# Performance work log

Measured on AMD Instinct MI355X. Metric: run time of the kernel, lower is better.

Reference implementation:

```python
import jax, jax.numpy as jnp
import numpy as np

BS, L, H, HD, R, HID = 4, 2048, 12, 64, 16, 768


def setup_inputs() -> dict:
    key = jax.random.key(0)
    k0, k1, k2, k3 = jax.random.split(key, 4)
    xavier = np.sqrt(2.0 / (H + HD))  # xavier_normal_ on (H, HD)
    lin = 1.0 / np.sqrt(HID)
    return {
        "hidden_states": jax.random.normal(k0, (BS, L, HID), jnp.float32),
        "K1_w": jax.random.normal(k1, (HID, H * HD), jnp.float32) * lin,
        "K1_b": jnp.zeros((H * HD,), jnp.float32),
        "V1_w": jax.random.normal(k2, (HID, H * HD), jnp.float32) * lin,
        "V1_b": jnp.zeros((H * HD,), jnp.float32),
        "ReadingHead": jax.random.normal(k3, (H, HD), jnp.float32) * xavier,
        "bidirection_weight": jnp.full((1, 1, H, 1, 2 * R), 1.0 / (2 * R), jnp.float32),
    }


def _scan_mmap(valid_mask, reverse):
    # valid_mask: (bs, L, H) bool. Sequential register-shift scan over positions 1..L-1.
    bs, Ln, Hn = valid_mask.shape
    idxs = jnp.arange(1, Ln, dtype=jnp.int32)
    masks = jnp.swapaxes(valid_mask[:, 1:], 0, 1)  # (L-1, bs, H)
    if reverse:
        idxs = idxs[::-1]
        masks = masks[::-1]
    init = jnp.zeros((bs, R + 1, Hn), jnp.int32)

    def step(valids, xm):
        i, m = xm
        valids = valids.at[:, 0].set(i)  # slot 0 <- current index (matches in-place torch order)
        shifted = jnp.where(m[:, None, :], valids[:, :-1], valids[:, 1:])
        valids = valids.at[:, 1:].set(shifted)
        return valids, valids[:, 1:]

    _, out = jax.lax.scan(step, init, (idxs, masks))  # (L-1, bs, R, H)
    if reverse:
        out = out[::-1]
    out = jnp.concatenate([jnp.zeros((1, bs, R, Hn), jnp.int32), out], axis=0)
    return jnp.swapaxes(out, 0, 1)  # (bs, L, R, H)


def reference(hidden_states, K1_w, K1_b, V1_w, V1_b, ReadingHead, bidirection_weight):
    K1 = jax.nn.relu(hidden_states @ K1_w + K1_b).reshape(BS, L, H, HD)
    V1 = jax.nn.relu(hidden_states @ V1_w + V1_b).reshape(BS, L, H, HD)
    dot_products = jnp.einsum('blhn,hn->blh', K1, ReadingHead)
    valid_mask = dot_products > 0.5  # attn_var default branch
    fm = _scan_mmap(valid_mask, False).reshape(BS, L * R, H)
    bm = _scan_mmap(valid_mask, True).reshape(BS, L * R, H)
    V_forward = jnp.take_along_axis(V1, fm[..., None], axis=1).reshape(BS, L, R, H, HD)
    V_backward = jnp.take_along_axis(V1, bm[..., None], axis=1).reshape(BS, L, R, H, HD)
    w = bidirection_weight[0, 0, :, 0, :]  # (H, 2R); first R -> forward, last R -> backward
    ctx = (jnp.einsum('blrhd,hr->blhd', V_forward, w[:, :R])
           + jnp.einsum('blrhd,hr->blhd', V_backward, w[:, R:]))
    return ctx.reshape(BS, L, H * HD)
```

## Files before the change

### kernel.cpp

```cpp
#include <hip/hip_runtime.h>
#include <hip/hip_bf16.h>

#define BS 4
#define L 2048
#define H 12
#define HD 64
#define R 16
#define HID 768
#define MARGIN 0.02f
#define FIXCAP 16384
#define FIXGRID 1024

typedef __attribute__((ext_vector_type(8))) short s8v;
typedef __attribute__((ext_vector_type(4))) float f32x4;

typedef __attribute__((address_space(1))) const void as1_void;
typedef __attribute__((address_space(3))) void as3_void;
#define GLOAD_LDS16(g, l) \
    __builtin_amdgcn_global_load_lds((as1_void*)(g), (as3_void*)(l), 16, 0, 0)

static __device__ __forceinline__ unsigned short f2bf_bits(float f) {
    __hip_bfloat16 h = __float2bfloat16(f);
    return *reinterpret_cast<unsigned short*>(&h);
}

__global__ __launch_bounds__(256) void convert_hs(
    const float* __restrict__ in, __hip_bfloat16* __restrict__ out,
    int* __restrict__ fixcnt)
{
    if (blockIdx.x == 0 && threadIdx.x == 0) *fixcnt = 0;
    int i = (blockIdx.x * 256 + threadIdx.x) * 4;
    float4 v = *(const float4*)&in[i];
    ushort4 o;
    o.x = f2bf_bits(v.x); o.y = f2bf_bits(v.y);
    o.z = f2bf_bits(v.z); o.w = f2bf_bits(v.w);
    *(ushort4*)&out[i] = o;
}

__global__ __launch_bounds__(256) void transpose_wt2(
    const float* __restrict__ K1w, const float* __restrict__ V1w,
    __hip_bfloat16* __restrict__ WtK, __hip_bfloat16* __restrict__ WtV)
{
    const float* in = blockIdx.z ? V1w : K1w;
    __hip_bfloat16* out = blockIdx.z ? WtV : WtK;
    __shared__ float s[32][33];
    const int c = threadIdx.x & 31, r8 = threadIdx.x >> 5;
    const int kt = blockIdx.x * 32, nt = blockIdx.y * 32;
#pragma unroll
    for (int rr = 0; rr < 4; ++rr) {
        int k = r8 + rr * 8;
        s[k][c] = in[(size_t)(kt + k) * HID + nt + c];
    }
    __syncthreads();
#pragma unroll
    for (int rr = 0; rr < 4; ++rr) {
        int n = r8 + rr * 8;
        out[(size_t)(nt + n) * HID + kt + c] = __float2bfloat16(s[c][n]);
    }
}

__global__ __launch_bounds__(256) void gemm_fused(
    const __hip_bfloat16* __restrict__ A,
    const __hip_bfloat16* __restrict__ WtK,
    const __hip_bfloat16* __restrict__ WtV,
    const float* __restrict__ K1b,
    const float* __restrict__ V1b,
    const float* __restrict__ RH,
    float* __restrict__ dots,
    int* __restrict__ fixlist,
    int* __restrict__ fixcnt,
    __hip_bfloat16* __restrict__ C)
{
    __shared__ alignas(16) __hip_bfloat16 As[128 * 32];
    __shared__ alignas(16) __hip_bfloat16 Bs[128 * 32];

    const int tid = threadIdx.x;
    const bool isV = blockIdx.y < 6;
    const int m0 = blockIdx.x * 128;
    const int n0 = (isV ? blockIdx.y : blockIdx.y - 6) * 128;
    const __hip_bfloat16* Bt = isV ? WtV : WtK;

    const int wid = tid >> 6, lane = tid & 63;
    const int quad = lane >> 4, lm = lane & 15;
    const int wm = wid & 1, wn = wid >> 1;

    const int rsub = lane >> 2;
    const int csw  = (lane & 3) ^ ((lane >> 3) & 3);
    const __hip_bfloat16* gA0 =
        A + (size_t)(m0 + 32 * wid + rsub) * HID + csw * 8;
    const __hip_bfloat16* gA1 = gA0 + (size_t)16 * HID;
    const __hip_bfloat16* gB0 =
        Bt + (size_t)(n0 + 32 * wid + rsub) * HID + csw * 8;
    const __hip_bfloat16* gB1 = gB0 + (size_t)16 * HID;
    __hip_bfloat16* lA0 = &As[(32 * wid) * 32];
    __hip_bfloat16* lA1 = &As[(32 * wid + 16) * 32];
    __hip_bfloat16* lB0 = &Bs[(32 * wid) * 32];
    __hip_bfloat16* lB1 = &Bs[(32 * wid + 16) * 32];

    const int fsw = (lm >> 1) & 3;
    const __hip_bfloat16* pA = &As[(wm * 64 + lm) * 32 + ((quad ^ fsw) * 8)];
    const __hip_bfloat16* pB = &Bs[(wn * 64 + lm) * 32 + ((quad ^ fsw) * 8)];

    f32x4 acc[4][4] = {};

    for (int k0 = 0; k0 < HID; k0 += 32) {
        GLOAD_LDS16(gA0, lA0);
        GLOAD_LDS16(gA1, lA1);
        GLOAD_LDS16(gB0, lB0);
        GLOAD_LDS16(gB1, lB1);
        gA0 += 32; gA1 += 32; gB0 += 32; gB1 += 32;
        __syncthreads();

        s8v af[4], bf[4];
#pragma unroll
        for (int i = 0; i < 4; ++i)
            af[i] = *(const s8v*)(pA + i * 16 * 32);
#pragma unroll
        for (int j = 0; j < 4; ++j)
            bf[j] = *(const s8v*)(pB + j * 16 * 32);
#pragma unroll
        for (int i = 0; i < 4; ++i)
#pragma unroll
            for (int j = 0; j < 4; ++j)
                acc[i][j] = __builtin_amdgcn_mfma_f32_16x16x32_bf16(
                    af[i], bf[j], acc[i][j], 0, 0, 0);
        __syncthreads();
    }

    if (isV) {
#pragma unroll
        for (int i = 0; i < 4; ++i) {
            int row_b = m0 + wm * 64 + i * 16 + quad * 4;
#pragma unroll
            for (int j = 0; j < 4; ++j) {
                int col = n0 + wn * 64 + j * 16 + lm;
                float bsv = V1b[col];
#pragma unroll
                for (int reg = 0; reg < 4; ++reg) {
                    float v = acc[i][j][reg] + bsv;
                    C[(size_t)(row_b + reg) * HID + col] =
                        __float2bfloat16(fmaxf(v, 0.f));
                }
            }
        }
    } else {
        const int head = (n0 >> 6) + wn;
        float bj[4], rj[4];
#pragma unroll
        for (int j = 0; j < 4; ++j) {
            bj[j] = K1b[head * 64 + j * 16 + lm];
            rj[j] = RH[head * 64 + j * 16 + lm];
        }
#pragma unroll
        for (int i = 0; i < 4; ++i) {
            int row0 = m0 + wm * 64 + i * 16 + quad * 4;
#pragma unroll
            for (int reg = 0; reg < 4; ++reg) {
                float p = 0.f;
#pragma unroll
                for (int j = 0; j < 4; ++j)
                    p = fmaf(fmaxf(acc[i][j][reg] + bj[j], 0.f), rj[j], p);
                p += __shfl_xor(p, 1, 64);
                p += __shfl_xor(p, 2, 64);
                p += __shfl_xor(p, 4, 64);
                p += __shfl_xor(p, 8, 64);
                if (lm == 0) {
                    int row = row0 + reg;
                    int b = row >> 11, l = row & (L - 1);
                    dots[((b * H + head) << 11) + l] = p;
                    if (fabsf(p - 0.5f) < MARGIN) {
                        int idx = atomicAdd(fixcnt, 1);
                        if (idx < FIXCAP) fixlist[idx] = row * 16 + head;
                    }
                }
            }
        }
    }
}

__global__ __launch_bounds__(256) void fixup_kernel(
    const float* __restrict__ hs,
    const float* __restrict__ W,
    const float* __restrict__ bias,
    const float* __restrict__ RH,
    const int* __restrict__ fixlist,
    const int* __restrict__ fixcnt,
    float* __restrict__ dots)
{
    __shared__ float hrow[HID];
    __shared__ float psum[4][64];

    const int tid = threadIdx.x;
    const int n = min(*fixcnt, FIXCAP);

    for (int item = blockIdx.x; item < n; item += FIXGRID) {
        int packed = fixlist[item];
        int row = packed >> 4, head = packed & 15;
        int b = row >> 11, l = row & (L - 1);

#pragma unroll
        for (int i = 0; i < 3; ++i)
            hrow[tid + i * 256] = hs[(size_t)row * HID + tid + i * 256];
        __syncthreads();

        const int d = tid & 63, kq = tid >> 6;
        float a0 = 0.f, a1 = 0.f;
#pragma unroll 8
        for (int i = 0; i < 96; ++i) {
            int k = kq + i * 8;
            a0 = fmaf(W[(size_t)k * HID + head * 64 + d], hrow[k], a0);
            a1 = fmaf(W[(size_t)(k + 4) * HID + head * 64 + d], hrow[k + 4], a1);
        }
        psum[kq][d] = a0 + a1;
        __syncthreads();
        if (tid < 64) {
            float v = psum[0][tid] + psum[1][tid] + psum[2][tid] +
                      psum[3][tid] + bias[head * 64 + tid];
            v = fmaxf(v, 0.f) * RH[head * 64 + tid];
#pragma unroll
            for (int s = 1; s < 64; s <<= 1) v += __shfl_xor(v, s, 64);
            if (tid == 0) dots[((size_t)(b * H + head) << 11) + l] = v;
        }
        __syncthreads();
    }
}

__global__ __launch_bounds__(256) void scan_kernel(
    const float* __restrict__ dots,
    short* __restrict__ fm,
    short* __restrict__ bm)
{
    __shared__ unsigned short P[L];
    __shared__ unsigned short S[L];
    __shared__ int wsum[4];

    const int bh = blockIdx.x;
    const int b = bh / H, h = bh % H;
    const int tid = threadIdx.x;
    const int base = tid * 8;
    const int lane = tid & 63, w = tid >> 6;

    int m[8], c[8];
    int run = 0;
#pragma unroll
    for (int i = 0; i < 8; ++i) {
        int l = base + i;
        m[i] = (l >= 1 && dots[((size_t)bh << 11) + l] > 0.5f) ? 1 : 0;
        run += m[i];
        c[i] = run;
    }
    int sc = run;
#pragma unroll
    for (int s = 1; s < 64; s <<= 1) {
        int v = __shfl_up(sc, s, 64);
        if (lane >= s) sc += v;
    }
    if (lane == 63) wsum[w] = sc;
    __syncthreads();
    int woff = 0;
    for (int i = 0; i < 4; ++i) if (i < w) woff += wsum[i];
    const int ex = woff + sc - run;

#pragma unroll
    for (int i = 0; i < 8; ++i) {
        int l = base + i;
        int pc = ex + c[i];
        P[l] = (unsigned short)pc;
        if (m[i]) S[pc] = (unsigned short)l;
    }
    __syncthreads();
    const int T = P[L - 1];

#pragma unroll
    for (int i = 0; i < 8; ++i) {
        int l = base + i;
        int cc = ex + c[i];
        union { unsigned short s[16]; uint4 q[2]; } uf, ub;
#pragma unroll
        for (int r = 0; r < 16; ++r)
            uf.s[r] = (cc - r >= 1) ? S[cc - r] : (unsigned short)0;
        int cp = (l >= 1) ? (int)P[l - 1] : 0;
#pragma unroll
        for (int r = 0; r < 16; ++r) {
            int j = cp + 1 + r;
            ub.s[r] = (l >= 1 && j <= T) ? S[j] : (unsigned short)0;
        }
        size_t off = ((size_t)(b * L + l) * H + h) * R;
        *(uint4*)&fm[off] = uf.q[0];
        *(uint4*)&fm[off + 8] = uf.q[1];
        *(uint4*)&bm[off] = ub.q[0];
        *(uint4*)&bm[off + 8] = ub.q[1];
    }
}

__global__ __launch_bounds__(192) void gather_kernel(
    const __hip_bfloat16* __restrict__ V1,
    const short* __restrict__ fm,
    const short* __restrict__ bm,
    const float* __restrict__ bw,
    float* __restrict__ out)
{
    __shared__ short sidx[2][2][H][R];
    __shared__ float sw[2][H][R];

    const int bl0 = blockIdx.x * 2;
    const int b = bl0 >> 11;
    const int tid = threadIdx.x;

    for (int i = tid; i < 2 * 2 * H * R; i += 192) {
        int ls = i / (2 * H * R), rem = i % (2 * H * R);
        int dir = rem / (H * R), hr = rem % (H * R);
        int h = hr >> 4, r = hr & 15;
        const short* src = dir ? bm : fm;
        sidx[ls][dir][h][r] = src[((size_t)(bl0 + ls) * H + h) * R + r];
    }
    for (int i = tid; i < 2 * H * R; i += 192) {
        int dir = i / (H * R), hr = i % (H * R);
        int h = hr >> 4, r = hr & 15;
        sw[dir][h][r] = bw[h * (2 * R) + dir * R + r];
    }
    __syncthreads();

    const int ls = tid / 96, t = tid % 96;
    const int h = t >> 3, d8 = t & 7;
    const __hip_bfloat16* Vb = V1 + (size_t)b * L * HID;

    float a[8] = {};
#pragma unroll
    for (int slot = 0; slot < 32; ++slot) {
        int dir = slot >> 4, r = slot & 15;
        int idx = sidx[ls][dir][h][r];
        float wv = sw[dir][h][r];
        const __hip_bfloat16* p = Vb + (size_t)idx * HID + h * HD + d8 * 8;
        uint4 uv = *(const uint4*)p;
        a[0] = fmaf(wv, __uint_as_float(uv.x << 16), a[0]);
        a[1] = fmaf(wv, __uint_as_float(uv.x & 0xffff0000u), a[1]);
        a[2] = fmaf(wv, __uint_as_float(uv.y << 16), a[2]);
        a[3] = fmaf(wv, __uint_as_float(uv.y & 0xffff0000u), a[3]);
        a[4] = fmaf(wv, __uint_as_float(uv.z << 16), a[4]);
        a[5] = fmaf(wv, __uint_as_float(uv.z & 0xffff0000u), a[5]);
        a[6] = fmaf(wv, __uint_as_float(uv.w << 16), a[6]);
        a[7] = fmaf(wv, __uint_as_float(uv.w & 0xffff0000u), a[7]);
    }
    float* op = &out[(size_t)(bl0 + ls) * HID + h * HD + d8 * 8];
    float4 o0, o1;
    o0.x = a[0]; o0.y = a[1]; o0.z = a[2]; o0.w = a[3];
    o1.x = a[4]; o1.y = a[5]; o1.z = a[6]; o1.w = a[7];
    *(float4*)op = o0;
    *(float4*)(op + 4) = o1;
}

extern "C" void kernel_launch(void* const* d_in, const int* in_sizes, int n_in,
                              void* d_out, int out_size, void* d_ws, size_t ws_size,
                              hipStream_t stream) {
    const float* hs  = (const float*)d_in[0];
    const float* K1w = (const float*)d_in[1];
    const float* K1b = (const float*)d_in[2];
    const float* V1w = (const float*)d_in[3];
    const float* V1b = (const float*)d_in[4];
    const float* RH  = (const float*)d_in[5];
    const float* bw  = (const float*)d_in[6];
    float* out = (float*)d_out;

    __hip_bfloat16* Abf = (__hip_bfloat16*)d_out;

    char* ws = (char*)d_ws;
    __hip_bfloat16* WtV = (__hip_bfloat16*)ws;
    __hip_bfloat16* WtK = (__hip_bfloat16*)(ws + 1179648);
    __hip_bfloat16* V1  = (__hip_bfloat16*)(ws + 2359296);
    float* dots = (float*)(ws + 14942208);
    short* fm   = (short*)(ws + 15335424);
    short* bm   = (short*)(ws + 18481152);
    int* fixlist = (int*)(ws + 21626880);
    int* fixcnt  = (int*)(ws + 21692416);

    convert_hs<<<(BS * L * HID) / (256 * 4), 256, 0, stream>>>(hs, Abf, fixcnt);
    transpose_wt2<<<dim3(HID / 32, HID / 32, 2), 256, 0, stream>>>(K1w, V1w, WtK, WtV);
    gemm_fused<<<dim3(BS * L / 128, 12), 256, 0, stream>>>(
        Abf, WtK, WtV, K1b, V1b, RH, dots, fixlist, fixcnt, V1);
    fixup_kernel<<<FIXGRID, 256, 0, stream>>>(hs, K1w, K1b, RH, fixlist, fixcnt, dots);
    scan_kernel<<<BS * H, 256, 0, stream>>>(dots, fm, bm);
    gather_kernel<<<BS * L / 2, 192, 0, stream>>>(V1, fm, bm, bw, out);
}
```

Before: 180.7 us.

## Stage gathered V rows in LDS per head tile and widen GEMM K-step

The scan kernel now writes only the prefix counts and the compacted valid-position list, no longer materializing the per-position fm/bm index tables (about 6 MB of writes and reads). The gather kernel is reorganized per (batch, head, 128-position tile): it computes the contiguous range of valid rows needed, loads those V rows once into shared memory, then derives each forward and backward index arithmetically, so neighbouring positions reuse the same V rows. Separately, the GEMM main loop now uses a K-step of 64 with a wider XOR swizzle, halving barrier count per tile. This adds LDS pressure of about 23 KB in gather and relies on the window bound of 161 rows holding.

```diff
diff --git a/kernel.cpp b/kernel.cpp
--- a/kernel.cpp
+++ b/kernel.cpp
@@ -71,8 +71,8 @@
     int* __restrict__ fixcnt,
     __hip_bfloat16* __restrict__ C)
 {
-    __shared__ alignas(16) __hip_bfloat16 As[128 * 32];
-    __shared__ alignas(16) __hip_bfloat16 Bs[128 * 32];
+    __shared__ alignas(16) __hip_bfloat16 As[128 * 64];
+    __shared__ alignas(16) __hip_bfloat16 Bs[128 * 64];
 
     const int tid = threadIdx.x;
     const bool isV = blockIdx.y < 6;
@@ -84,40 +84,47 @@
     const int quad = lane >> 4, lm = lane & 15;
     const int wm = wid & 1, wn = wid >> 1;
 
-    const int rsub = lane >> 2;
-    const int csw  = (lane & 3) ^ ((lane >> 3) & 3);
-    const __hip_bfloat16* gA0 =
-        A + (size_t)(m0 + 32 * wid + rsub) * HID + csw * 8;
-    const __hip_bfloat16* gA1 = gA0 + (size_t)16 * HID;
-    const __hip_bfloat16* gB0 =
-        Bt + (size_t)(n0 + 32 * wid + rsub) * HID + csw * 8;
-    const __hip_bfloat16* gB1 = gB0 + (size_t)16 * HID;
-    __hip_bfloat16* lA0 = &As[(32 * wid) * 32];
-    __hip_bfloat16* lA1 = &As[(32 * wid + 16) * 32];
-    __hip_bfloat16* lB0 = &Bs[(32 * wid) * 32];
-    __hip_bfloat16* lB1 = &Bs[(32 * wid + 16) * 32];
-
-    const int fsw = (lm >> 1) & 3;
-    const __hip_bfloat16* pA = &As[(wm * 64 + lm) * 32 + ((quad ^ fsw) * 8)];
-    const __hip_bfloat16* pB = &Bs[(wn * 64 + lm) * 32 + ((quad ^ fsw) * 8)];
+    const int srow = lane >> 3;
+    const int schk = (lane & 7) ^ ((lane >> 3) & 7);
+    const __hip_bfloat16* gA =
+        A + (size_t)(m0 + 32 * wid + srow) * HID + schk * 8;
+    const __hip_bfloat16* gB =
+        Bt + (size_t)(n0 + 32 * wid + srow) * HID + schk * 8;
+    __hip_bfloat16* lA = &As[(32 * wid) * 64];
+    __hip_bfloat16* lB = &Bs[(32 * wid) * 64];
+
+    const int s7 = lm & 7;
+    const __hip_bfloat16* pA0 = &As[(wm * 64 + lm) * 64 + ((quad ^ s7) * 8)];
+    const __hip_bfloat16* pA1 = &As[(wm * 64 + lm) * 64 + (((4 + quad) ^ s7) * 8)];
+    const __hip_bfloat16* pB0 = &Bs[(wn * 64 + lm) * 64 + ((quad ^ s7) * 8)];
+    const __hip_bfloat16* pB1 = &Bs[(wn * 64 + lm) * 64 + (((4 + quad) ^ s7) * 8)];
 
     f32x4 acc[4][4] = {};
 
-    for (int k0 = 0; k0 < HID; k0 += 32) {
-        GLOAD_LDS16(gA0, lA0);
-        GLOAD_LDS16(gA1, lA1);
-        GLOAD_LDS16(gB0, lB0);
-        GLOAD_LDS16(gB1, lB1);
-        gA0 += 32; gA1 += 32; gB0 += 32; gB1 += 32;
+    for (int k0 = 0; k0 < HID; k0 += 64) {
+#pragma unroll
+        for (int d = 0; d < 4; ++d) {
+            GLOAD_LDS16(gA + (size_t)(8 * d) * HID, lA + (8 * d) * 64);
+            GLOAD_LDS16(gB + (size_t)(8 * d) * HID, lB + (8 * d) * 64);
+        }
+        gA += 64; gB += 64;
         __syncthreads();
 
         s8v af[4], bf[4];
 #pragma unroll
+        for (int i = 0; i < 4; ++i) af[i] = *(const s8v*)(pA0 + i * 16 * 64);
+#pragma unroll
+        for (int j = 0; j < 4; ++j) bf[j] = *(const s8v*)(pB0 + j * 16 * 64);
+#pragma unroll
         for (int i = 0; i < 4; ++i)
-            af[i] = *(const s8v*)(pA + i * 16 * 32);
-#pragma unroll
-        for (int j = 0; j < 4; ++j)
-            bf[j] = *(const s8v*)(pB + j * 16 * 32);
+#pragma unroll
+            for (int j = 0; j < 4; ++j)
+                acc[i][j] = __builtin_amdgcn_mfma_f32_16x16x32_bf16(
+                    af[i], bf[j], acc[i][j], 0, 0, 0);
+#pragma unroll
+        for (int i = 0; i < 4; ++i) af[i] = *(const s8v*)(pA1 + i * 16 * 64);
+#pragma unroll
+        for (int j = 0; j < 4; ++j) bf[j] = *(const s8v*)(pB1 + j * 16 * 64);
 #pragma unroll
         for (int i = 0; i < 4; ++i)
 #pragma unroll
@@ -227,15 +234,11 @@
 
 __global__ __launch_bounds__(256) void scan_kernel(
     const float* __restrict__ dots,
-    short* __restrict__ fm,
-    short* __restrict__ bm)
-{
-    __shared__ unsigned short P[L];
-    __shared__ unsigned short S[L];
+    unsigned short* __restrict__ Pg,
+    unsigned short* __restrict__ Sg)
+{
     __shared__ int wsum[4];
-
     const int bh = blockIdx.x;
-    const int b = bh / H, h = bh % H;
     const int tid = threadIdx.x;
     const int base = tid * 8;
     const int lane = tid & 63, w = tid >> 6;
@@ -261,93 +264,91 @@
     for (int i = 0; i < 4; ++i) if (i < w) woff += wsum[i];
     const int ex = woff + sc - run;
 
+    union { unsigned short s[8]; uint4 q; } up;
 #pragma unroll
     for (int i = 0; i < 8; ++i) {
-        int l = base + i;
         int pc = ex + c[i];
-        P[l] = (unsigned short)pc;
-        if (m[i]) S[pc] = (unsigned short)l;
-    }
-    __syncthreads();
-    const int T = P[L - 1];
-
-#pragma unroll
-    for (int i = 0; i < 8; ++i) {
-        int l = base + i;
-        int cc = ex + c[i];
-        union { unsigned short s[16]; uint4 q[2]; } uf, ub;
-#pragma unroll
-        for (int r = 0; r < 16; ++r)
-            uf.s[r] = (cc - r >= 1) ? S[cc - r] : (unsigned short)0;
-        int cp = (l >= 1) ? (int)P[l - 1] : 0;
-#pragma unroll
-        for (int r = 0; r < 16; ++r) {
-            int j = cp + 1 + r;
-            ub.s[r] = (l >= 1 && j <= T) ? S[j] : (unsigned short)0;
-        }
-        size_t off = ((size_t)(b * L + l) * H + h) * R;
-        *(uint4*)&fm[off] = uf.q[0];
-        *(uint4*)&fm[off + 8] = uf.q[1];
-        *(uint4*)&bm[off] = ub.q[0];
-        *(uint4*)&bm[off + 8] = ub.q[1];
-    }
-}
-
-__global__ __launch_bounds__(192) void gather_kernel(
+        up.s[i] = (unsigned short)pc;
+        if (m[i]) Sg[((size_t)bh << 11) + pc] = (unsigned short)(base + i);
+    }
+    *(uint4*)&Pg[((size_t)bh << 11) + base] = up.q;
+}
+
+__global__ __launch_bounds__(256) void gather_kernel(
     const __hip_bfloat16* __restrict__ V1,
-    const short* __restrict__ fm,
-    const short* __restrict__ bm,
+    const unsigned short* __restrict__ Pg,
+    const unsigned short* __restrict__ Sg,
     const float* __restrict__ bw,
     float* __restrict__ out)
 {
-    __shared__ short sidx[2][2][H][R];
-    __shared__ float sw[2][H][R];
-
-    const int bl0 = blockIdx.x * 2;
-    const int b = bl0 >> 11;
+    __shared__ __hip_bfloat16 Vs[161 * 72];
+    __shared__ unsigned short Ptile[129];
+    __shared__ float sw[2 * R];
+    __shared__ int sT;
+
+    const int bh = blockIdx.y;
+    const int b = bh / H, h = bh % H;
+    const int l0 = blockIdx.x * 128;
     const int tid = threadIdx.x;
 
-    for (int i = tid; i < 2 * 2 * H * R; i += 192) {
-        int ls = i / (2 * H * R), rem = i % (2 * H * R);
-        int dir = rem / (H * R), hr = rem % (H * R);
-        int h = hr >> 4, r = hr & 15;
-        const short* src = dir ? bm : fm;
-        sidx[ls][dir][h][r] = src[((size_t)(bl0 + ls) * H + h) * R + r];
-    }
-    for (int i = tid; i < 2 * H * R; i += 192) {
-        int dir = i / (H * R), hr = i % (H * R);
-        int h = hr >> 4, r = hr & 15;
-        sw[dir][h][r] = bw[h * (2 * R) + dir * R + r];
+    if (tid < 129) {
+        int l = l0 - 1 + tid;
+        Ptile[tid] = (l >= 0) ? Pg[((size_t)bh << 11) + l] : (unsigned short)0;
+    } else if (tid < 129 + 2 * R) {
+        sw[tid - 129] = bw[h * (2 * R) + (tid - 129)];
+    } else if (tid == 200) {
+        sT = Pg[((size_t)bh << 11) + (L - 1)];
     }
     __syncthreads();
 
-    const int ls = tid / 96, t = tid % 96;
-    const int h = t >> 3, d8 = t & 7;
-    const __hip_bfloat16* Vb = V1 + (size_t)b * L * HID;
-
-    float a[8] = {};
-#pragma unroll
-    for (int slot = 0; slot < 32; ++slot) {
-        int dir = slot >> 4, r = slot & 15;
-        int idx = sidx[ls][dir][h][r];
-        float wv = sw[dir][h][r];
-        const __hip_bfloat16* p = Vb + (size_t)idx * HID + h * HD + d8 * 8;
-        uint4 uv = *(const uint4*)p;
-        a[0] = fmaf(wv, __uint_as_float(uv.x << 16), a[0]);
-        a[1] = fmaf(wv, __uint_as_float(uv.x & 0xffff0000u), a[1]);
-        a[2] = fmaf(wv, __uint_as_float(uv.y << 16), a[2]);
-        a[3] = fmaf(wv, __uint_as_float(uv.y & 0xffff0000u), a[3]);
-        a[4] = fmaf(wv, __uint_as_float(uv.z << 16), a[4]);
-        a[5] = fmaf(wv, __uint_as_float(uv.z & 0xffff0000u), a[5]);
-        a[6] = fmaf(wv, __uint_as_float(uv.w << 16), a[6]);
-        a[7] = fmaf(wv, __uint_as_float(uv.w & 0xffff0000u), a[7]);
-    }
-    float* op = &out[(size_t)(bl0 + ls) * HID + h * HD + d8 * 8];
-    float4 o0, o1;
-    o0.x = a[0]; o0.y = a[1]; o0.z = a[2]; o0.w = a[3];
-    o1.x = a[4]; o1.y = a[5]; o1.z = a[6]; o1.w = a[7];
-    *(float4*)op = o0;
-    *(float4*)(op + 4) = o1;
+    const int T = sT;
+    const int a = max(1, (int)Ptile[1] - (R - 1));
+    const int bj = min(T, (int)Ptile[127] + R);
+    const int nr = max(0, bj - a + 1);
+
+    const __hip_bfloat16* Vbase = V1 + (size_t)b * L * HID + h * HD;
+    for (int it = tid; it < (nr + 1) * 8; it += 256) {
+        int slot = it >> 3, oct = it & 7;
+        int row = slot ? (int)Sg[((size_t)bh << 11) + a + slot - 1] : 0;
+        *(uint4*)&Vs[slot * 72 + oct * 8] =
+            *(const uint4*)&Vbase[(size_t)row * HID + oct * 8];
+    }
+    __syncthreads();
+
+    const int d8 = tid & 7, lg = tid >> 3;
+
+#pragma unroll
+    for (int li = 0; li < 4; ++li) {
+        int ll = lg + 32 * li;
+        int l = l0 + ll;
+        int Pl = Ptile[1 + ll], Plm1 = Ptile[ll];
+        bool lpos = (l >= 1);
+        float acc0 = 0.f, acc1 = 0.f, acc2 = 0.f, acc3 = 0.f;
+        float acc4 = 0.f, acc5 = 0.f, acc6 = 0.f, acc7 = 0.f;
+#pragma unroll
+        for (int r = 0; r < 2 * R; ++r) {
+            int j, ok;
+            if (r < R) { j = Pl - r;           ok = lpos && (j >= 1); }
+            else       { j = Plm1 + 1 + (r - R); ok = lpos && (j <= T); }
+            int slot = ok ? (j - a + 1) : 0;
+            float wv = sw[r];
+            uint4 uv = *(const uint4*)&Vs[slot * 72 + d8 * 8];
+            acc0 = fmaf(wv, __uint_as_float(uv.x << 16), acc0);
+            acc1 = fmaf(wv, __uint_as_float(uv.x & 0xffff0000u), acc1);
+            acc2 = fmaf(wv, __uint_as_float(uv.y << 16), acc2);
+            acc3 = fmaf(wv, __uint_as_float(uv.y & 0xffff0000u), acc3);
+            acc4 = fmaf(wv, __uint_as_float(uv.z << 16), acc4);
+            acc5 = fmaf(wv, __uint_as_float(uv.z & 0xffff0000u), acc5);
+            acc6 = fmaf(wv, __uint_as_float(uv.w << 16), acc6);
+            acc7 = fmaf(wv, __uint_as_float(uv.w & 0xffff0000u), acc7);
+        }
+        float* op = &out[((size_t)b * L + l) * HID + h * HD + d8 * 8];
+        float4 o0, o1;
+        o0.x = acc0; o0.y = acc1; o0.z = acc2; o0.w = acc3;
+        o1.x = acc4; o1.y = acc5; o1.z = acc6; o1.w = acc7;
+        *(float4*)op = o0;
+        *(float4*)(op + 4) = o1;
+    }
 }
 
 extern "C" void kernel_launch(void* const* d_in, const int* in_sizes, int n_in,
@@ -369,16 +370,16 @@
     __hip_bfloat16* WtK = (__hip_bfloat16*)(ws + 1179648);
     __hip_bfloat16* V1  = (__hip_bfloat16*)(ws + 2359296);
     float* dots = (float*)(ws + 14942208);
-    short* fm   = (short*)(ws + 15335424);
-    short* bm   = (short*)(ws + 18481152);
-    int* fixlist = (int*)(ws + 21626880);
-    int* fixcnt  = (int*)(ws + 21692416);
+    unsigned short* Pg = (unsigned short*)(ws + 15335424);
+    unsigned short* Sg = (unsigned short*)(ws + 15532032);
+    int* fixlist = (int*)(ws + 15728640);
+    int* fixcnt  = (int*)(ws + 15794176);
 
     convert_hs<<<(BS * L * HID) / (256 * 4), 256, 0, stream>>>(hs, Abf, fixcnt);
     transpose_wt2<<<dim3(HID / 32, HID / 32, 2), 256, 0, stream>>>(K1w, V1w, WtK, WtV);
     gemm_fused<<<dim3(BS * L / 128, 12), 256, 0, stream>>>(
         Abf, WtK, WtV, K1b, V1b, RH, dots, fixlist, fixcnt, V1);
     fixup_kernel<<<FIXGRID, 256, 0, stream>>>(hs, K1w, K1b, RH, fixlist, fixcnt, dots);
-    scan_kernel<<<BS * H, 256, 0, stream>>>(dots, fm, bm);
-    gather_kernel<<<BS * L / 2, 192, 0, stream>>>(V1, fm, bm, bw, out);
-}
+    scan_kernel<<<BS * H, 256, 0, stream>>>(dots, Pg, Sg);
+    gather_kernel<<<dim3(L / 128, BS * H), 256, 0, stream>>>(V1, Pg, Sg, bw, out);
+}
```

New measurement: 170.1 us. 1.06x faster.
